# Performance work log

Hardware: AMD Instinct MI355X
Metric: run time of the kernel (lower is better)

Reference implementation:

```python
import jax, jax.numpy as jnp
import numpy as np

B, S, D, H = 2, 2048, 1024, 16
DK = D // H  # 64, per-head key/value dim


def setup_inputs() -> dict:
    key = jax.random.key(0)
    ks = jax.random.split(key, 8)
    q = jax.random.normal(ks[0], (B, S, D), dtype=jnp.float32)
    k = jax.random.normal(ks[1], (B, S, D), dtype=jnp.float32)
    v = jax.random.normal(ks[2], (B, S, D), dtype=jnp.float32)
    # per-head projection weights, initialized like torch.randn in the original
    W_q = jax.random.normal(ks[3], (H, D, DK), dtype=jnp.float32)
    W_k = jax.random.normal(ks[4], (H, D, DK), dtype=jnp.float32)
    W_v = jax.random.normal(ks[5], (H, D, DK), dtype=jnp.float32)
    # output nn.Linear(H*DK, D): weight [D, H*DK], bias [D]
    bound = 1.0 / np.sqrt(H * DK)
    W_o = jax.random.uniform(ks[6], (D, H * DK), dtype=jnp.float32, minval=-bound, maxval=bound)
    b_o = jax.random.uniform(ks[7], (D,), dtype=jnp.float32, minval=-bound, maxval=bound)
    return {"q": q, "k": k, "v": v, "W_q": W_q, "W_k": W_k, "W_v": W_v, "W_o": W_o, "b_o": b_o}


def reference(q, k, v, W_q, W_k, W_v, W_o, b_o):
    dk = W_q.shape[-1]
    # batched per-head projections (replaces the Python loop over heads)
    qh = jnp.einsum('bsd,hdk->bhsk', q, W_q)  # [B,H,S,DK]
    kh = jnp.einsum('bsd,hdk->bhsk', k, W_k)
    vh = jnp.einsum('bsd,hdk->bhsk', v, W_v)
    scale = jnp.asarray(np.sqrt(dk), qh.dtype)
    scores = jnp.einsum('bhsk,bhtk->bhst', qh, kh) / scale  # [B,H,S,S]
    attn = jax.nn.softmax(scores, axis=-1)
    ctx = jnp.einsum('bhst,bhtk->bhsk', attn, vh)  # [B,H,S,DK]
    # concat heads along feature dim (matches torch.cat(..., dim=2))
    b, h, s, d = ctx.shape
    ctx = ctx.transpose(0, 2, 1, 3).reshape(b, s, h * d)  # [B,S,H*DK]
    return ctx @ W_o.T + b_o  # [B,S,D]
```

## Files before the change

### kernel.cpp

```cpp
#include <hip/hip_runtime.h>
#include <math.h>

#define B_ 2
#define S_ 2048
#define D_ 1024
#define H_ 16
#define ATTN_C 0.18033688011f

typedef unsigned short ushort_t;
typedef __attribute__((ext_vector_type(8))) short short8;
typedef __attribute__((ext_vector_type(4))) short short4v;
typedef __attribute__((ext_vector_type(4))) float f32x4;
typedef __attribute__((ext_vector_type(2))) float f32x2;
typedef __attribute__((ext_vector_type(16))) float f32x16;
typedef __attribute__((ext_vector_type(4))) unsigned int uint4v;

#define MFMA(A, B, C) __builtin_amdgcn_mfma_f32_32x32x16_bf16((A), (B), (C), 0, 0, 0)
#define Z16 {0.f,0.f,0.f,0.f,0.f,0.f,0.f,0.f,0.f,0.f,0.f,0.f,0.f,0.f,0.f,0.f}

__device__ __forceinline__ ushort_t bf16rn(float x) {
    unsigned int u = __builtin_bit_cast(unsigned int, x);
    u += 0x7FFFu + ((u >> 16) & 1u);
    return (ushort_t)(u >> 16);
}
__device__ __forceinline__ float bf16tof(ushort_t h) {
    return __builtin_bit_cast(float, (unsigned int)h << 16);
}
__device__ __forceinline__ unsigned cvtpk(float lo, float hi) {
    unsigned r;
    asm("v_cvt_pk_bf16_f32 %0, %1, %2" : "=v"(r) : "v"(lo), "v"(hi));
    return r;
}
__device__ __forceinline__ void gload16(const void* g, void* l) {
    __builtin_amdgcn_global_load_lds(
        (const __attribute__((address_space(1))) unsigned int*)(unsigned long long)g,
        (__attribute__((address_space(3))) unsigned int*)(unsigned int)(unsigned long long)l,
        16, 0, 0);
}

__global__ __launch_bounds__(256) void cvtx_kernel(
    const float* __restrict__ Xq, const float* __restrict__ Xk,
    const float* __restrict__ Xv,
    ushort_t* __restrict__ Xh, ushort_t* __restrict__ Xl)
{
    const int pr = blockIdx.y;
    const float* X = pr == 0 ? Xq : pr == 1 ? Xk : Xv;
    const size_t idx = ((size_t)blockIdx.x * 256 + threadIdx.x) * 8;
    f32x4 v0 = *(const f32x4*)(X + idx);
    f32x4 v1 = *(const f32x4*)(X + idx + 4);
    float f[8] = {v0.x, v0.y, v0.z, v0.w, v1.x, v1.y, v1.z, v1.w};
    short8 hi, lo;
#pragma unroll
    for (int i = 0; i < 8; ++i) {
        ushort_t hh = bf16rn(f[i]);
        hi[i] = (short)hh;
        lo[i] = (short)bf16rn(f[i] - bf16tof(hh));
    }
    const size_t base = (size_t)pr * 2 * S_ * D_;
    *(short8*)(Xh + base + idx) = hi;
    if (pr < 2) *(short8*)(Xl + base + idx) = lo;
}

__global__ __launch_bounds__(256) void cvtw_kernel(
    const float* __restrict__ Wq, const float* __restrict__ Wk,
    const float* __restrict__ Wv,
    ushort_t* __restrict__ wqh, ushort_t* __restrict__ wql,
    ushort_t* __restrict__ wkh, ushort_t* __restrict__ wkl,
    ushort_t* __restrict__ wvh)
{
    __shared__ float T[64][68];
    const int dt = blockIdx.x, h = blockIdx.y, mat = blockIdx.z;
    const int tid = threadIdx.x;
    const float* W = mat == 0 ? Wq : mat == 1 ? Wk : Wv;
    const float* Wb = W + ((size_t)h * 1024 + dt * 64) * 64;
#pragma unroll
    for (int u = 0; u < 4; ++u) {
        int idx = tid + u * 256;
        int d = idx >> 4, c4 = idx & 15;
        f32x4 v = *(const f32x4*)(Wb + (size_t)d * 64 + c4 * 4);
        T[d][c4 * 4 + 0] = v.x; T[d][c4 * 4 + 1] = v.y;
        T[d][c4 * 4 + 2] = v.z; T[d][c4 * 4 + 3] = v.w;
    }
    __syncthreads();
    ushort_t* oh = mat == 0 ? wqh : mat == 1 ? wkh : wvh;
    ushort_t* ol = mat == 0 ? wql : mat == 1 ? wkl : nullptr;
#pragma unroll
    for (int u = 0; u < 4; ++u) {
        int idx = tid + u * 256;
        int n = idx >> 4, c4 = idx & 15;
        float v0 = T[c4 * 4 + 0][n], v1 = T[c4 * 4 + 1][n];
        float v2 = T[c4 * 4 + 2][n], v3 = T[c4 * 4 + 3][n];
        ushort_t h0 = bf16rn(v0), h1 = bf16rn(v1), h2 = bf16rn(v2), h3 = bf16rn(v3);
        size_t off = ((size_t)h * 64 + n) * 1024 + dt * 64 + c4 * 4;
        short4v hv = {(short)h0, (short)h1, (short)h2, (short)h3};
        *(short4v*)(oh + off) = hv;
        if (ol) {
            short4v lv = {(short)bf16rn(v0 - bf16tof(h0)), (short)bf16rn(v1 - bf16tof(h1)),
                          (short)bf16rn(v2 - bf16tof(h2)), (short)bf16rn(v3 - bf16tof(h3))};
            *(short4v*)(ol + off) = lv;
        }
    }
}

__global__ __launch_bounds__(256) void cvtwo_kernel(
    const float* __restrict__ Wo, ushort_t* __restrict__ wob)
{
    size_t idx = (size_t)blockIdx.x * 256 + threadIdx.x;
    f32x4 v = *(const f32x4*)(Wo + idx * 4);
    short4v o = {(short)bf16rn(v.x), (short)bf16rn(v.y),
                 (short)bf16rn(v.z), (short)bf16rn(v.w)};
    *(short4v*)(wob + idx * 4) = o;
}

__global__ __launch_bounds__(256, 2) void proj_kernel(
    const ushort_t* __restrict__ Xh, const ushort_t* __restrict__ Xl,
    const ushort_t* __restrict__ Wh_q, const ushort_t* __restrict__ Wl_q,
    const ushort_t* __restrict__ Wh_k, const ushort_t* __restrict__ Wl_k,
    const ushort_t* __restrict__ Wh_v,
    ushort_t* __restrict__ Oq_h, ushort_t* __restrict__ Oq_l,
    ushort_t* __restrict__ Ok_h, ushort_t* __restrict__ Ok_l,
    ushort_t* __restrict__ Ovt)
{
    __shared__ __align__(16) ushort_t Xs[128 * 128];
    __shared__ __align__(16) ushort_t Ws[128 * 128];
    const int tid = threadIdx.x;
    const int wv = tid >> 6, lane = tid & 63;
    const int lo32 = lane & 31, g = lane >> 5;
    const int wm = wv >> 1, wn = wv & 1;
    const int lrow = lane >> 4, lg = lane & 15;
    const int m0 = blockIdx.x * 128;
    const int n0 = blockIdx.y * 128;
    const int pr = blockIdx.z >> 1, b = blockIdx.z & 1;
    const bool split = (pr != 2);
    const ushort_t* Whp = pr == 0 ? Wh_q : pr == 1 ? Wh_k : Wh_v;
    const ushort_t* Wlp = pr == 0 ? Wl_q : pr == 1 ? Wl_k : Wh_v;
    const ushort_t* Xhb = Xh + ((size_t)(pr * 2 + b) * S_ + m0) * D_;
    const ushort_t* Xlb = Xl + ((size_t)(pr * 2 + b) * S_ + m0) * D_;
    f32x16 a00 = Z16, a01 = Z16, a10 = Z16, a11 = Z16;

    for (int d0 = 0; d0 < D_; d0 += 64) {
        __syncthreads();
#pragma unroll
        for (int u = 0; u < 8; ++u) {
            int row = u * 16 + wv * 4 + lrow;
            int gs = lg ^ (row & 15);
            int half = gs >> 3, c8 = gs & 7;
            const ushort_t* srcX = ((half && split) ? Xlb : Xhb) + (size_t)row * D_ + d0 + c8 * 8;
            gload16(srcX, (char*)Xs + (u * 16 + wv * 4) * 256);
            const ushort_t* srcW = ((half && split) ? Wlp : Whp) + (size_t)(n0 + row) * 1024 + d0 + c8 * 8;
            gload16(srcW, (char*)Ws + (u * 16 + wv * 4) * 256);
        }
        __syncthreads();
#pragma unroll
        for (int ks = 0; ks < 4; ++ks) {
            int coff = ks * 16 + g * 8;
            int r0 = wm * 64 + lo32, r1 = r0 + 32;
            int c0 = wn * 64 + lo32, c1 = c0 + 32;
            short8 a0h = *(const short8*)&Xs[(r0 * 128 + coff) ^ ((r0 & 15) << 3)];
            short8 a1h = *(const short8*)&Xs[(r1 * 128 + coff) ^ ((r1 & 15) << 3)];
            short8 b0h = *(const short8*)&Ws[(c0 * 128 + coff) ^ ((c0 & 15) << 3)];
            short8 b1h = *(const short8*)&Ws[(c1 * 128 + coff) ^ ((c1 & 15) << 3)];
            a00 = MFMA(a0h, b0h, a00);
            a01 = MFMA(a0h, b1h, a01);
            a10 = MFMA(a1h, b0h, a10);
            a11 = MFMA(a1h, b1h, a11);
            if (split) {
                short8 a0l = *(const short8*)&Xs[(r0 * 128 + 64 + coff) ^ ((r0 & 15) << 3)];
                short8 a1l = *(const short8*)&Xs[(r1 * 128 + 64 + coff) ^ ((r1 & 15) << 3)];
                short8 b0l = *(const short8*)&Ws[(c0 * 128 + 64 + coff) ^ ((c0 & 15) << 3)];
                short8 b1l = *(const short8*)&Ws[(c1 * 128 + 64 + coff) ^ ((c1 & 15) << 3)];
                a00 = MFMA(a0h, b0l, a00); a00 = MFMA(a0l, b0h, a00);
                a01 = MFMA(a0h, b1l, a01); a01 = MFMA(a0l, b1h, a01);
                a10 = MFMA(a1h, b0l, a10); a10 = MFMA(a1l, b0h, a10);
                a11 = MFMA(a1h, b1l, a11); a11 = MFMA(a1l, b1h, a11);
            }
        }
    }
    ushort_t* OH = pr == 0 ? Oq_h : pr == 1 ? Ok_h : Ovt;
    ushort_t* OL = pr == 0 ? Oq_l : pr == 1 ? Ok_l : Ovt;
    const bool qscale = (pr == 0);
#define PROJ_STORE(ACC, MT, NT)                                               \
    _Pragma("unroll")                                                         \
    for (int r = 0; r < 16; ++r) {                                            \
        int s_loc = m0 + wm * 64 + (MT) * 32 + (r & 3) + 8 * (r >> 2) + 4 * g;\
        int col = n0 + wn * 64 + (NT) * 32 + lo32;                            \
        int hh_ = col >> 6, nn = col & 63;                                    \
        float val = ACC[r];                                                   \
        if (qscale) val *= ATTN_C;                                            \
        if (split) {                                                          \
            size_t off = (((size_t)b * H_ + hh_) * S_ + s_loc) * 64 + nn;     \
            ushort_t hv = bf16rn(val);                                        \
            OH[off] = hv;                                                     \
            OL[off] = bf16rn(val - bf16tof(hv));                              \
        } else {                                                              \
            size_t offt = (((size_t)b * H_ + hh_) * 64 + nn) * S_ + s_loc;    \
            OH[offt] = bf16rn(val);                                           \
        }                                                                     \
    }
    PROJ_STORE(a00, 0, 0)
    PROJ_STORE(a01, 0, 1)
    PROJ_STORE(a10, 1, 0)
    PROJ_STORE(a11, 1, 1)
#undef PROJ_STORE
}

__global__ __launch_bounds__(256, 2) void attn_kernel(
    const ushort_t* __restrict__ qh_h, const ushort_t* __restrict__ qh_l,
    const ushort_t* __restrict__ kh_h, const ushort_t* __restrict__ kh_l,
    const ushort_t* __restrict__ vt, ushort_t* __restrict__ Opart,
    float* __restrict__ Ml)
{
    __shared__ __align__(16) char smem[49152];
    ushort_t* Ks = (ushort_t*)smem;
    ushort_t* Vt = (ushort_t*)(smem + 32768);
    const int tid = threadIdx.x;
    const int wv = tid >> 6, lane = tid & 63;
    const int lo32 = lane & 31, g = lane >> 5;
    const int lrow = lane >> 4, lg = lane & 15;
    const int s0 = blockIdx.x * 256;
    const int h = blockIdx.y;
    const int b = blockIdx.z >> 1, sp = blockIdx.z & 1;
    const size_t bhs = ((size_t)b * H_ + h) * S_ * 64;

    short8 qfh[2][4], qfl[2][4];
#pragma unroll
    for (int c = 0; c < 2; ++c) {
        const ushort_t* Qrh = qh_h + bhs + (size_t)(s0 + wv * 64 + c * 32 + lo32) * 64;
        const ushort_t* Qrl = qh_l + bhs + (size_t)(s0 + wv * 64 + c * 32 + lo32) * 64;
#pragma unroll
        for (int ks = 0; ks < 4; ++ks) {
            qfh[c][ks] = *(const short8*)(Qrh + ks * 16 + g * 8);
            qfl[c][ks] = *(const short8*)(Qrl + ks * 16 + g * 8);
        }
    }
    const ushort_t* Kgh = kh_h + bhs;
    const ushort_t* Kgl = kh_l + bhs;
    const ushort_t* Vtg = vt + ((size_t)b * H_ + h) * 64 * S_;

    f32x16 o00 = Z16, o01 = Z16, o10 = Z16, o11 = Z16;
    float mrun0 = -3.0e38f, mrun1 = -3.0e38f;
    float lrun0 = 0.f, lrun1 = 0.f;
    const int kvbeg = sp * (S_ / 2), kvend = kvbeg + (S_ / 2);

    for (int kv0 = kvbeg; kv0 < kvend; kv0 += 128) {
        __syncthreads();
#pragma unroll
        for (int u = 0; u < 8; ++u) {
            int row = u * 16 + wv * 4 + lrow;
            int gs = lg ^ (row & 15);
            int half = gs >> 3, c8 = gs & 7;
            const ushort_t* src = (half ? Kgl : Kgh) + (size_t)(kv0 + row) * 64 + c8 * 8;
            gload16(src, (char*)Ks + (u * 16 + wv * 4) * 256);
        }
#pragma unroll
        for (int u = 0; u < 4; ++u) {
            int d = u * 16 + wv * 4 + lrow;
            int gsrc = (lg & 8) | ((lg & 7) ^ (d & 7));
            const ushort_t* src = Vtg + (size_t)d * S_ + kv0 + gsrc * 8;
            gload16(src, (char*)Vt + (u * 16 + wv * 4) * 256);
        }
        __syncthreads();
#pragma unroll 1
        for (int ch = 0; ch < 4; ++ch) {
            const int kvb = ch * 32;
            const int krow = kvb + lo32;
            const int ksw = (krow & 15) << 3;
            short8 kfh0 = *(const short8*)&Ks[(krow * 128 + 0 * 16 + g * 8) ^ ksw];
            short8 kfh1 = *(const short8*)&Ks[(krow * 128 + 1 * 16 + g * 8) ^ ksw];
            short8 kfh2 = *(const short8*)&Ks[(krow * 128 + 2 * 16 + g * 8) ^ ksw];
            short8 kfh3 = *(const short8*)&Ks[(krow * 128 + 3 * 16 + g * 8) ^ ksw];
            f32x16 st0 = Z16, st1 = Z16;
            st0 = MFMA(kfh0, qfh[0][0], st0);  st1 = MFMA(kfh0, qfh[1][0], st1);
            st0 = MFMA(kfh1, qfh[0][1], st0);  st1 = MFMA(kfh1, qfh[1][1], st1);
            st0 = MFMA(kfh2, qfh[0][2], st0);  st1 = MFMA(kfh2, qfh[1][2], st1);
            st0 = MFMA(kfh3, qfh[0][3], st0);  st1 = MFMA(kfh3, qfh[1][3], st1);
            float cm0 = fmaxf(fmaxf(fmaxf(st0[0], st0[1]), fmaxf(st0[2], st0[3])),
                              fmaxf(fmaxf(st0[4], st0[5]), fmaxf(st0[6], st0[7])));
            cm0 = fmaxf(cm0, fmaxf(fmaxf(fmaxf(st0[8], st0[9]), fmaxf(st0[10], st0[11])),
                                   fmaxf(fmaxf(st0[12], st0[13]), fmaxf(st0[14], st0[15]))));
            float cm1 = fmaxf(fmaxf(fmaxf(st1[0], st1[1]), fmaxf(st1[2], st1[3])),
                              fmaxf(fmaxf(st1[4], st1[5]), fmaxf(st1[6], st1[7])));
            cm1 = fmaxf(cm1, fmaxf(fmaxf(fmaxf(st1[8], st1[9]), fmaxf(st1[10], st1[11])),
                                   fmaxf(fmaxf(st1[12], st1[13]), fmaxf(st1[14], st1[15]))));
            cm0 = fmaxf(cm0, __shfl_xor(cm0, 32));
            cm1 = fmaxf(cm1, __shfl_xor(cm1, 32));
            const bool need0 = !__all(cm0 <= mrun0 - 142.f);
            const bool need1 = !__all(cm1 <= mrun1 - 142.f);
            if (!need0 && !need1) continue;
            short8 kfl0 = *(const short8*)&Ks[(krow * 128 + 64 + 0 * 16 + g * 8) ^ ksw];
            short8 kfl1 = *(const short8*)&Ks[(krow * 128 + 64 + 1 * 16 + g * 8) ^ ksw];
            short8 kfl2 = *(const short8*)&Ks[(krow * 128 + 64 + 2 * 16 + g * 8) ^ ksw];
            short8 kfl3 = *(const short8*)&Ks[(krow * 128 + 64 + 3 * 16 + g * 8) ^ ksw];
            unsigned pw0[8], pw1[8];
            if (need0) {
                st0 = MFMA(kfh0, qfl[0][0], st0);  st0 = MFMA(kfl0, qfh[0][0], st0);
                st0 = MFMA(kfh1, qfl[0][1], st0);  st0 = MFMA(kfl1, qfh[0][1], st0);
                st0 = MFMA(kfh2, qfl[0][2], st0);  st0 = MFMA(kfl2, qfh[0][2], st0);
                st0 = MFMA(kfh3, qfl[0][3], st0);  st0 = MFMA(kfl3, qfh[0][3], st0);
                float cme = fmaxf(fmaxf(fmaxf(st0[0], st0[1]), fmaxf(st0[2], st0[3])),
                                  fmaxf(fmaxf(st0[4], st0[5]), fmaxf(st0[6], st0[7])));
                cme = fmaxf(cme, fmaxf(fmaxf(fmaxf(st0[8], st0[9]), fmaxf(st0[10], st0[11])),
                                       fmaxf(fmaxf(st0[12], st0[13]), fmaxf(st0[14], st0[15]))));
                cme = fmaxf(cme, __shfl_xor(cme, 32));
                if (!__all(cme <= mrun0)) {
                    float mnew = fmaxf(mrun0, cme);
                    float corr = __builtin_amdgcn_exp2f(mrun0 - mnew);
                    lrun0 *= corr;
#pragma unroll
                    for (int r = 0; r < 16; ++r) { o00[r] *= corr; o01[r] *= corr; }
                    mrun0 = mnew;
                }
                float p[16], ls = 0.f;
#pragma unroll
                for (int r = 0; r < 16; ++r) {
                    p[r] = __builtin_amdgcn_exp2f(st0[r] - mrun0);
                    ls += p[r];
                }
                lrun0 += ls;
#pragma unroll
                for (int ks2 = 0; ks2 < 2; ++ks2) {
                    unsigned w0 = cvtpk(p[ks2 * 8 + 0], p[ks2 * 8 + 1]);
                    unsigned w1 = cvtpk(p[ks2 * 8 + 2], p[ks2 * 8 + 3]);
                    unsigned w2 = cvtpk(p[ks2 * 8 + 4], p[ks2 * 8 + 5]);
                    unsigned w3 = cvtpk(p[ks2 * 8 + 6], p[ks2 * 8 + 7]);
                    asm("v_permlane32_swap_b32 %0, %1" : "+v"(w0), "+v"(w2));
                    asm("v_permlane32_swap_b32 %0, %1" : "+v"(w1), "+v"(w3));
                    pw0[ks2 * 4 + 0] = w0; pw0[ks2 * 4 + 1] = w1;
                    pw0[ks2 * 4 + 2] = w2; pw0[ks2 * 4 + 3] = w3;
                }
            }
            if (need1) {
                st1 = MFMA(kfh0, qfl[1][0], st1);  st1 = MFMA(kfl0, qfh[1][0], st1);
                st1 = MFMA(kfh1, qfl[1][1], st1);  st1 = MFMA(kfl1, qfh[1][1], st1);
                st1 = MFMA(kfh2, qfl[1][2], st1);  st1 = MFMA(kfl2, qfh[1][2], st1);
                st1 = MFMA(kfh3, qfl[1][3], st1);  st1 = MFMA(kfl3, qfh[1][3], st1);
                float cme = fmaxf(fmaxf(fmaxf(st1[0], st1[1]), fmaxf(st1[2], st1[3])),
                                  fmaxf(fmaxf(st1[4], st1[5]), fmaxf(st1[6], st1[7])));
                cme = fmaxf(cme, fmaxf(fmaxf(fmaxf(st1[8], st1[9]), fmaxf(st1[10], st1[11])),
                                       fmaxf(fmaxf(st1[12], st1[13]), fmaxf(st1[14], st1[15]))));
                cme = fmaxf(cme, __shfl_xor(cme, 32));
                if (!__all(cme <= mrun1)) {
                    float mnew = fmaxf(mrun1, cme);
                    float corr = __builtin_amdgcn_exp2f(mrun1 - mnew);
                    lrun1 *= corr;
#pragma unroll
                    for (int r = 0; r < 16; ++r) { o10[r] *= corr; o11[r] *= corr; }
                    mrun1 = mnew;
                }
                float p[16], ls = 0.f;
#pragma unroll
                for (int r = 0; r < 16; ++r) {
                    p[r] = __builtin_amdgcn_exp2f(st1[r] - mrun1);
                    ls += p[r];
                }
                lrun1 += ls;
#pragma unroll
                for (int ks2 = 0; ks2 < 2; ++ks2) {
                    unsigned w0 = cvtpk(p[ks2 * 8 + 0], p[ks2 * 8 + 1]);
                    unsigned w1 = cvtpk(p[ks2 * 8 + 2], p[ks2 * 8 + 3]);
                    unsigned w2 = cvtpk(p[ks2 * 8 + 4], p[ks2 * 8 + 5]);
                    unsigned w3 = cvtpk(p[ks2 * 8 + 6], p[ks2 * 8 + 7]);
                    asm("v_permlane32_swap_b32 %0, %1" : "+v"(w0), "+v"(w2));
                    asm("v_permlane32_swap_b32 %0, %1" : "+v"(w1), "+v"(w3));
                    pw1[ks2 * 4 + 0] = w0; pw1[ks2 * 4 + 1] = w1;
                    pw1[ks2 * 4 + 2] = w2; pw1[ks2 * 4 + 3] = w3;
                }
            }
#pragma unroll
            for (int ks2 = 0; ks2 < 2; ++ks2) {
                int kvf = kvb + ks2 * 16 + g * 8;
                int vsw = (lo32 & 7) << 3;
                short8 vf0 = *(const short8*)&Vt[(lo32 * 128 + kvf) ^ vsw];
                short8 vf1 = *(const short8*)&Vt[((lo32 + 32) * 128 + kvf) ^ vsw];
                if (need0) {
                    uint4v a = {pw0[ks2 * 4 + 0], pw0[ks2 * 4 + 1],
                                pw0[ks2 * 4 + 2], pw0[ks2 * 4 + 3]};
                    short8 pf = __builtin_bit_cast(short8, a);
                    o00 = MFMA(vf0, pf, o00);
                    o01 = MFMA(vf1, pf, o01);
                }
                if (need1) {
                    uint4v a = {pw1[ks2 * 4 + 0], pw1[ks2 * 4 + 1],
                                pw1[ks2 * 4 + 2], pw1[ks2 * 4 + 3]};
                    short8 pf = __builtin_bit_cast(short8, a);
                    o10 = MFMA(vf0, pf, o10);
                    o11 = MFMA(vf1, pf, o11);
                }
            }
        }
    }
    lrun0 += __shfl_xor(lrun0, 32);
    lrun1 += __shfl_xor(lrun1, 32);
    __syncthreads();
    float* Oe = ((float*)smem) + wv * 2048;
    const size_t orowb = (size_t)sp * (B_ * H_ * S_) + ((size_t)b * H_ + h) * S_ + s0 + wv * 64;
#pragma unroll
    for (int r = 0; r < 16; ++r) {
        int dd = (r & 3) + 8 * (r >> 2) + 4 * g;
        int qsw = (lo32 & 7) << 2;
        Oe[(lo32 * 64 + dd) ^ qsw] = o00[r];
        Oe[(lo32 * 64 + 32 + dd) ^ qsw] = o01[r];
    }
#pragma unroll
    for (int rep = 0; rep < 8; ++rep) {
        int idx = lane + rep * 64;
        int qq = idx >> 4, d4 = idx & 15;
        f32x4 ov = *(const f32x4*)&Oe[(qq * 64 + d4 * 4) ^ ((qq & 7) << 2)];
        short4v pk4 = {(short)bf16rn(ov.x), (short)bf16rn(ov.y),
                       (short)bf16rn(ov.z), (short)bf16rn(ov.w)};
        *(short4v*)(Opart + (orowb + qq) * 64 + d4 * 4) = pk4;
    }
    if (g == 0) {
        f32x2 ml = {mrun0, lrun0};
        *(f32x2*)(Ml + (orowb + lo32) * 2) = ml;
    }
    __builtin_amdgcn_s_waitcnt(0);
#pragma unroll
    for (int r = 0; r < 16; ++r) {
        int dd = (r & 3) + 8 * (r >> 2) + 4 * g;
        int qsw = (lo32 & 7) << 2;
        Oe[(lo32 * 64 + dd) ^ qsw] = o10[r];
        Oe[(lo32 * 64 + 32 + dd) ^ qsw] = o11[r];
    }
#pragma unroll
    for (int rep = 0; rep < 8; ++rep) {
        int idx = lane + rep * 64;
        int qq = idx >> 4, d4 = idx & 15;
        f32x4 ov = *(const f32x4*)&Oe[(qq * 64 + d4 * 4) ^ ((qq & 7) << 2)];
        short4v pk4 = {(short)bf16rn(ov.x), (short)bf16rn(ov.y),
                       (short)bf16rn(ov.z), (short)bf16rn(ov.w)};
        *(short4v*)(Opart + (orowb + 32 + qq) * 64 + d4 * 4) = pk4;
    }
    if (g == 0) {
        f32x2 ml = {mrun1, lrun1};
        *(f32x2*)(Ml + (orowb + 32 + lo32) * 2) = ml;
    }
}

__global__ __launch_bounds__(256) void merge_kernel(
    const ushort_t* __restrict__ Opart, const float* __restrict__ Ml,
    ushort_t* __restrict__ ctxb)
{
    const int NROW = B_ * H_ * S_;
    int gidx = blockIdx.x * 256 + threadIdx.x;
    int row = gidx >> 3, d8 = (gidx & 7) * 8;
    f32x2 ml0 = *(const f32x2*)(Ml + (size_t)row * 2);
    f32x2 ml1 = *(const f32x2*)(Ml + ((size_t)NROW + row) * 2);
    float M = fmaxf(ml0.x, ml1.x);
    float w0 = __builtin_amdgcn_exp2f(ml0.x - M);
    float w1 = __builtin_amdgcn_exp2f(ml1.x - M);
    float inv = 1.f / (ml0.y * w0 + ml1.y * w1);
    w0 *= inv; w1 *= inv;
    short8 a = *(const short8*)(Opart + (size_t)row * 64 + d8);
    short8 c = *(const short8*)(Opart + ((size_t)NROW + row) * 64 + d8);
    short8 o;
#pragma unroll
    for (int i = 0; i < 8; ++i) {
        float f = bf16tof((ushort_t)a[i]) * w0 + bf16tof((ushort_t)c[i]) * w1;
        o[i] = (short)bf16rn(f);
    }
    int bb = row >> 15, hh = (row >> 11) & 15, s = row & 2047;
    *(short8*)(ctxb + ((size_t)bb * S_ + s) * D_ + hh * 64 + d8) = o;
}

__global__ __launch_bounds__(128, 2) void outproj_kernel(
    const ushort_t* __restrict__ ctxb, const ushort_t* __restrict__ wob,
    const float* __restrict__ bo, float* __restrict__ Out)
{
    __shared__ __align__(16) ushort_t Cs[128 * 128];
    __shared__ __align__(16) ushort_t Ws2[64 * 128];
    const int tid = threadIdx.x;
    const int wv = tid >> 6, lane = tid & 63;
    const int lo32 = lane & 31, g = lane >> 5;
    const int lrow = lane >> 4, lg = lane & 15;
    const int n0 = blockIdx.x * 64;
    const int m0 = blockIdx.y * 128;
    f32x16 a00 = Z16, a01 = Z16, a10 = Z16, a11 = Z16;
    for (int k0 = 0; k0 < D_; k0 += 128) {
        __syncthreads();
#pragma unroll
        for (int u = 0; u < 16; ++u) {
            int row = u * 8 + wv * 4 + lrow;
            int gs = lg ^ (row & 15);
            const ushort_t* src = ctxb + (size_t)(m0 + row) * D_ + k0 + gs * 8;
            gload16(src, (char*)Cs + (u * 8 + wv * 4) * 256);
        }
#pragma unroll
        for (int u = 0; u < 8; ++u) {
            int row = u * 8 + wv * 4 + lrow;
            int gs = lg ^ (row & 15);
            const ushort_t* src = wob + (size_t)(n0 + row) * D_ + k0 + gs * 8;
            gload16(src, (char*)Ws2 + (u * 8 + wv * 4) * 256);
        }
        __syncthreads();
#pragma unroll
        for (int ks = 0; ks < 8; ++ks) {
            int coff = ks * 16 + g * 8;
            int r0 = wv * 64 + lo32, r1 = r0 + 32;
            int n1 = lo32 + 32;
            short8 A0 = *(const short8*)&Cs[(r0 * 128 + coff) ^ ((r0 & 15) << 3)];
            short8 A1 = *(const short8*)&Cs[(r1 * 128 + coff) ^ ((r1 & 15) << 3)];
            short8 B0 = *(const short8*)&Ws2[(lo32 * 128 + coff) ^ ((lo32 & 15) << 3)];
            short8 B1 = *(const short8*)&Ws2[(n1 * 128 + coff) ^ ((n1 & 15) << 3)];
            a00 = MFMA(A0, B0, a00);
            a01 = MFMA(A0, B1, a01);
            a10 = MFMA(A1, B0, a10);
            a11 = MFMA(A1, B1, a11);
        }
    }
    float b0v = bo[n0 + lo32], b1v = bo[n0 + 32 + lo32];
#define OUT_STORE(ACC, MT, NT, BV)                                          \
    _Pragma("unroll")                                                       \
    for (int r = 0; r < 16; ++r) {                                          \
        int m = m0 + wv * 64 + (MT) * 32 + (r & 3) + 8 * (r >> 2) + 4 * g;  \
        int n = n0 + (NT) * 32 + lo32;                                      \
        Out[(size_t)m * D_ + n] = ACC[r] + (BV);                            \
    }
    OUT_STORE(a00, 0, 0, b0v)
    OUT_STORE(a01, 0, 1, b1v)
    OUT_STORE(a10, 1, 0, b0v)
    OUT_STORE(a11, 1, 1, b1v)
#undef OUT_STORE
}

extern "C" void kernel_launch(void* const* d_in, const int* in_sizes, int n_in,
                              void* d_out, int out_size, void* d_ws,
                              size_t ws_size, hipStream_t stream)
{
    const float* q = (const float*)d_in[0];
    const float* k = (const float*)d_in[1];
    const float* v = (const float*)d_in[2];
    const float* W_q = (const float*)d_in[3];
    const float* W_k = (const float*)d_in[4];
    const float* W_v = (const float*)d_in[5];
    const float* W_o = (const float*)d_in[6];
    const float* b_o = (const float*)d_in[7];
    float* out = (float*)d_out;

    ushort_t* wqt_h = (ushort_t*)d_ws;
    ushort_t* wqt_l = wqt_h + (1 << 20);
    ushort_t* wkt_h = wqt_l + (1 << 20);
    ushort_t* wkt_l = wkt_h + (1 << 20);
    ushort_t* wvt_h = wkt_l + (1 << 20);
// ... 25 lines not shown
```

Baseline: 229.7 us.

## Load K fragments directly from global with register double-buffering, drop K LDS staging

K high/low fragments are no longer staged through shared memory. Each wave reads its K rows straight from global into registers, prefetching the next 32-row chunk while the current one computes. The low-part K is read from global only when the skip test says it is needed. The skip threshold moves from 142 to 150 and the four chunks per tile are fully unrolled. This lowers LDS use and cuts barrier-protected K copy traffic, but each wave now fetches K itself, so global/L2 traffic goes up, and the full unroll may raise register pressure.

```diff
diff --git a/kernel.cpp b/kernel.cpp
--- a/kernel.cpp
+++ b/kernel.cpp
@@ -210,9 +210,8 @@
     const ushort_t* __restrict__ vt, ushort_t* __restrict__ Opart,
     float* __restrict__ Ml)
 {
-    __shared__ __align__(16) char smem[49152];
-    ushort_t* Ks = (ushort_t*)smem;
-    ushort_t* Vt = (ushort_t*)(smem + 32768);
+    __shared__ __align__(16) char smem[32768];
+    ushort_t* Vt = (ushort_t*)smem;
     const int tid = threadIdx.x;
     const int wv = tid >> 6, lane = tid & 63;
     const int lo32 = lane & 31, g = lane >> 5;
@@ -240,18 +239,115 @@
     f32x16 o00 = Z16, o01 = Z16, o10 = Z16, o11 = Z16;
     float mrun0 = -3.0e38f, mrun1 = -3.0e38f;
     float lrun0 = 0.f, lrun1 = 0.f;
-    const int kvbeg = sp * (S_ / 2), kvend = kvbeg + (S_ / 2);
-
-    for (int kv0 = kvbeg; kv0 < kvend; kv0 += 128) {
+    const int kvbeg = sp * (S_ / 2);
+
+#define MAX16(ST) fmaxf(fmaxf(fmaxf(fmaxf(ST[0], ST[1]), fmaxf(ST[2], ST[3])),   \
+                              fmaxf(fmaxf(ST[4], ST[5]), fmaxf(ST[6], ST[7]))),  \
+                        fmaxf(fmaxf(fmaxf(ST[8], ST[9]), fmaxf(ST[10], ST[11])), \
+                              fmaxf(fmaxf(ST[12], ST[13]), fmaxf(ST[14], ST[15]))))
+
+#define SOFTMAX_PV(ST, MR, LR, OA, OB)                                        \
+    {                                                                         \
+        float cme = MAX16(ST);                                                \
+        cme = fmaxf(cme, __shfl_xor(cme, 32));                                \
+        if (!__all(cme <= MR)) {                                              \
+            float mnew = fmaxf(MR, cme);                                      \
+            float corr = __builtin_amdgcn_exp2f(MR - mnew);                   \
+            LR *= corr;                                                       \
+            _Pragma("unroll")                                                 \
+            for (int r = 0; r < 16; ++r) { OA[r] *= corr; OB[r] *= corr; }    \
+            MR = mnew;                                                        \
+        }                                                                     \
+        float p[16], ls = 0.f;                                                \
+        _Pragma("unroll")                                                     \
+        for (int r = 0; r < 16; ++r) {                                        \
+            p[r] = __builtin_amdgcn_exp2f(ST[r] - MR);                        \
+            ls += p[r];                                                       \
+        }                                                                     \
+        LR += ls;                                                             \
+        {                                                                     \
+            unsigned w0 = cvtpk(p[0], p[1]), w1 = cvtpk(p[2], p[3]);          \
+            unsigned w2 = cvtpk(p[4], p[5]), w3 = cvtpk(p[6], p[7]);          \
+            asm("v_permlane32_swap_b32 %0, %1" : "+v"(w0), "+v"(w2));         \
+            asm("v_permlane32_swap_b32 %0, %1" : "+v"(w1), "+v"(w3));         \
+            uint4v pa = {w0, w1, w2, w3};                                     \
+            short8 pf = __builtin_bit_cast(short8, pa);                       \
+            OA = MFMA(vfa0, pf, OA);                                          \
+            OB = MFMA(vfa1, pf, OB);                                          \
+            w0 = cvtpk(p[8], p[9]);  w1 = cvtpk(p[10], p[11]);                \
+            w2 = cvtpk(p[12], p[13]); w3 = cvtpk(p[14], p[15]);               \
+            asm("v_permlane32_swap_b32 %0, %1" : "+v"(w0), "+v"(w2));         \
+            asm("v_permlane32_swap_b32 %0, %1" : "+v"(w1), "+v"(w3));         \
+            uint4v pb = {w0, w1, w2, w3};                                     \
+            short8 pf2 = __builtin_bit_cast(short8, pb);                      \
+            OA = MFMA(vfb0, pf2, OA);                                         \
+            OB = MFMA(vfb1, pf2, OB);                                         \
+        }                                                                     \
+    }
+
+#define LOADK(CI, DST)                                                        \
+    {                                                                         \
+        int cc = (CI) > 31 ? 31 : (CI);                                       \
+        const ushort_t* pn = Kgh + (size_t)(kvbeg + cc * 32 + lo32) * 64 + g * 8; \
+        DST[0] = *(const short8*)(pn);                                        \
+        DST[1] = *(const short8*)(pn + 16);                                   \
+        DST[2] = *(const short8*)(pn + 32);                                   \
+        DST[3] = *(const short8*)(pn + 48);                                   \
+    }
+
+#define CHUNK_BODY(KC, KN, CI)                                                \
+    {                                                                         \
+        LOADK((CI) + 1, KN);                                                  \
+        f32x16 st0 = Z16, st1 = Z16;                                          \
+        st0 = MFMA(KC[0], qfh[0][0], st0);  st1 = MFMA(KC[0], qfh[1][0], st1);\
+        st0 = MFMA(KC[1], qfh[0][1], st0);  st1 = MFMA(KC[1], qfh[1][1], st1);\
+        st0 = MFMA(KC[2], qfh[0][2], st0);  st1 = MFMA(KC[2], qfh[1][2], st1);\
+        st0 = MFMA(KC[3], qfh[0][3], st0);  st1 = MFMA(KC[3], qfh[1][3], st1);\
+        float cm0 = MAX16(st0);                                               \
+        float cm1 = MAX16(st1);                                               \
+        cm0 = fmaxf(cm0, __shfl_xor(cm0, 32));                                \
+        cm1 = fmaxf(cm1, __shfl_xor(cm1, 32));                                \
+        const bool need0 = !__all(cm0 <= mrun0 - 150.f);                      \
+        const bool need1 = !__all(cm1 <= mrun1 - 150.f);                      \
+        if (need0 | need1) {                                                  \
+            const ushort_t* pl = Kgl + (size_t)(kvbeg + (CI) * 32 + lo32) * 64 + g * 8; \
+            short8 kl0 = *(const short8*)(pl);                                \
+            short8 kl1 = *(const short8*)(pl + 16);                           \
+            short8 kl2 = *(const short8*)(pl + 32);                           \
+            short8 kl3 = *(const short8*)(pl + 48);                           \
+            if (need0) {                                                      \
+                st0 = MFMA(KC[0], qfl[0][0], st0); st0 = MFMA(KC[1], qfl[0][1], st0); \
+                st0 = MFMA(KC[2], qfl[0][2], st0); st0 = MFMA(KC[3], qfl[0][3], st0); \
+            }                                                                 \
+            if (need1) {                                                      \
+                st1 = MFMA(KC[0], qfl[1][0], st1); st1 = MFMA(KC[1], qfl[1][1], st1); \
+                st1 = MFMA(KC[2], qfl[1][2], st1); st1 = MFMA(KC[3], qfl[1][3], st1); \
+            }                                                                 \
+            if (need0) {                                                      \
+                st0 = MFMA(kl0, qfh[0][0], st0); st0 = MFMA(kl1, qfh[0][1], st0); \
+                st0 = MFMA(kl2, qfh[0][2], st0); st0 = MFMA(kl3, qfh[0][3], st0); \
+            }                                                                 \
+            if (need1) {                                                      \
+                st1 = MFMA(kl0, qfh[1][0], st1); st1 = MFMA(kl1, qfh[1][1], st1); \
+                st1 = MFMA(kl2, qfh[1][2], st1); st1 = MFMA(kl3, qfh[1][3], st1); \
+            }                                                                 \
+            const int kvb = ((CI) & 3) * 32;                                  \
+            const int vsw = (lo32 & 7) << 3;                                  \
+            short8 vfa0 = *(const short8*)&Vt[(lo32 * 128 + kvb + g * 8) ^ vsw];        \
+            short8 vfa1 = *(const short8*)&Vt[((lo32 + 32) * 128 + kvb + g * 8) ^ vsw]; \
+            short8 vfb0 = *(const short8*)&Vt[(lo32 * 128 + kvb + 16 + g * 8) ^ vsw];   \
+            short8 vfb1 = *(const short8*)&Vt[((lo32 + 32) * 128 + kvb + 16 + g * 8) ^ vsw]; \
+            if (need0) SOFTMAX_PV(st0, mrun0, lrun0, o00, o01)                \
+            if (need1) SOFTMAX_PV(st1, mrun1, lrun1, o10, o11)                \
+        }                                                                     \
+    }
+
+    short8 kx[4], ky[4];
+    LOADK(0, kx);
+    int c = 0;
+    for (int t = 0; t < 8; ++t) {
+        const int kv0 = kvbeg + t * 128;
         __syncthreads();
-#pragma unroll
-        for (int u = 0; u < 8; ++u) {
-            int row = u * 16 + wv * 4 + lrow;
-            int gs = lg ^ (row & 15);
-            int half = gs >> 3, c8 = gs & 7;
-            const ushort_t* src = (half ? Kgl : Kgh) + (size_t)(kv0 + row) * 64 + c8 * 8;
-            gload16(src, (char*)Ks + (u * 16 + wv * 4) * 256);
-        }
 #pragma unroll
         for (int u = 0; u < 4; ++u) {
             int d = u * 16 + wv * 4 + lrow;
@@ -260,135 +356,17 @@
             gload16(src, (char*)Vt + (u * 16 + wv * 4) * 256);
         }
         __syncthreads();
-#pragma unroll 1
-        for (int ch = 0; ch < 4; ++ch) {
-            const int kvb = ch * 32;
-            const int krow = kvb + lo32;
-            const int ksw = (krow & 15) << 3;
-            short8 kfh0 = *(const short8*)&Ks[(krow * 128 + 0 * 16 + g * 8) ^ ksw];
-            short8 kfh1 = *(const short8*)&Ks[(krow * 128 + 1 * 16 + g * 8) ^ ksw];
-            short8 kfh2 = *(const short8*)&Ks[(krow * 128 + 2 * 16 + g * 8) ^ ksw];
-            short8 kfh3 = *(const short8*)&Ks[(krow * 128 + 3 * 16 + g * 8) ^ ksw];
-            f32x16 st0 = Z16, st1 = Z16;
-            st0 = MFMA(kfh0, qfh[0][0], st0);  st1 = MFMA(kfh0, qfh[1][0], st1);
-            st0 = MFMA(kfh1, qfh[0][1], st0);  st1 = MFMA(kfh1, qfh[1][1], st1);
-            st0 = MFMA(kfh2, qfh[0][2], st0);  st1 = MFMA(kfh2, qfh[1][2], st1);
-            st0 = MFMA(kfh3, qfh[0][3], st0);  st1 = MFMA(kfh3, qfh[1][3], st1);
-            float cm0 = fmaxf(fmaxf(fmaxf(st0[0], st0[1]), fmaxf(st0[2], st0[3])),
-                              fmaxf(fmaxf(st0[4], st0[5]), fmaxf(st0[6], st0[7])));
-            cm0 = fmaxf(cm0, fmaxf(fmaxf(fmaxf(st0[8], st0[9]), fmaxf(st0[10], st0[11])),
-                                   fmaxf(fmaxf(st0[12], st0[13]), fmaxf(st0[14], st0[15]))));
-            float cm1 = fmaxf(fmaxf(fmaxf(st1[0], st1[1]), fmaxf(st1[2], st1[3])),
-                              fmaxf(fmaxf(st1[4], st1[5]), fmaxf(st1[6], st1[7])));
-            cm1 = fmaxf(cm1, fmaxf(fmaxf(fmaxf(st1[8], st1[9]), fmaxf(st1[10], st1[11])),
-                                   fmaxf(fmaxf(st1[12], st1[13]), fmaxf(st1[14], st1[15]))));
-            cm0 = fmaxf(cm0, __shfl_xor(cm0, 32));
-            cm1 = fmaxf(cm1, __shfl_xor(cm1, 32));
-            const bool need0 = !__all(cm0 <= mrun0 - 142.f);
-            const bool need1 = !__all(cm1 <= mrun1 - 142.f);
-            if (!need0 && !need1) continue;
-            short8 kfl0 = *(const short8*)&Ks[(krow * 128 + 64 + 0 * 16 + g * 8) ^ ksw];
-            short8 kfl1 = *(const short8*)&Ks[(krow * 128 + 64 + 1 * 16 + g * 8) ^ ksw];
-            short8 kfl2 = *(const short8*)&Ks[(krow * 128 + 64 + 2 * 16 + g * 8) ^ ksw];
-            short8 kfl3 = *(const short8*)&Ks[(krow * 128 + 64 + 3 * 16 + g * 8) ^ ksw];
-            unsigned pw0[8], pw1[8];
-            if (need0) {
-                st0 = MFMA(kfh0, qfl[0][0], st0);  st0 = MFMA(kfl0, qfh[0][0], st0);
-                st0 = MFMA(kfh1, qfl[0][1], st0);  st0 = MFMA(kfl1, qfh[0][1], st0);
-                st0 = MFMA(kfh2, qfl[0][2], st0);  st0 = MFMA(kfl2, qfh[0][2], st0);
-                st0 = MFMA(kfh3, qfl[0][3], st0);  st0 = MFMA(kfl3, qfh[0][3], st0);
-                float cme = fmaxf(fmaxf(fmaxf(st0[0], st0[1]), fmaxf(st0[2], st0[3])),
-                                  fmaxf(fmaxf(st0[4], st0[5]), fmaxf(st0[6], st0[7])));
-                cme = fmaxf(cme, fmaxf(fmaxf(fmaxf(st0[8], st0[9]), fmaxf(st0[10], st0[11])),
-                                       fmaxf(fmaxf(st0[12], st0[13]), fmaxf(st0[14], st0[15]))));
-                cme = fmaxf(cme, __shfl_xor(cme, 32));
-                if (!__all(cme <= mrun0)) {
-                    float mnew = fmaxf(mrun0, cme);
-                    float corr = __builtin_amdgcn_exp2f(mrun0 - mnew);
-                    lrun0 *= corr;
-#pragma unroll
-                    for (int r = 0; r < 16; ++r) { o00[r] *= corr; o01[r] *= corr; }
-                    mrun0 = mnew;
-                }
-                float p[16], ls = 0.f;
-#pragma unroll
-                for (int r = 0; r < 16; ++r) {
-                    p[r] = __builtin_amdgcn_exp2f(st0[r] - mrun0);
-                    ls += p[r];
-                }
-                lrun0 += ls;
-#pragma unroll
-                for (int ks2 = 0; ks2 < 2; ++ks2) {
-                    unsigned w0 = cvtpk(p[ks2 * 8 + 0], p[ks2 * 8 + 1]);
-                    unsigned w1 = cvtpk(p[ks2 * 8 + 2], p[ks2 * 8 + 3]);
-                    unsigned w2 = cvtpk(p[ks2 * 8 + 4], p[ks2 * 8 + 5]);
-                    unsigned w3 = cvtpk(p[ks2 * 8 + 6], p[ks2 * 8 + 7]);
-                    asm("v_permlane32_swap_b32 %0, %1" : "+v"(w0), "+v"(w2));
-                    asm("v_permlane32_swap_b32 %0, %1" : "+v"(w1), "+v"(w3));
-                    pw0[ks2 * 4 + 0] = w0; pw0[ks2 * 4 + 1] = w1;
-                    pw0[ks2 * 4 + 2] = w2; pw0[ks2 * 4 + 3] = w3;
-                }
-            }
-            if (need1) {
-                st1 = MFMA(kfh0, qfl[1][0], st1);  st1 = MFMA(kfl0, qfh[1][0], st1);
-                st1 = MFMA(kfh1, qfl[1][1], st1);  st1 = MFMA(kfl1, qfh[1][1], st1);
-                st1 = MFMA(kfh2, qfl[1][2], st1);  st1 = MFMA(kfl2, qfh[1][2], st1);
-                st1 = MFMA(kfh3, qfl[1][3], st1);  st1 = MFMA(kfl3, qfh[1][3], st1);
-                float cme = fmaxf(fmaxf(fmaxf(st1[0], st1[1]), fmaxf(st1[2], st1[3])),
-                                  fmaxf(fmaxf(st1[4], st1[5]), fmaxf(st1[6], st1[7])));
-                cme = fmaxf(cme, fmaxf(fmaxf(fmaxf(st1[8], st1[9]), fmaxf(st1[10], st1[11])),
-                                       fmaxf(fmaxf(st1[12], st1[13]), fmaxf(st1[14], st1[15]))));
-                cme = fmaxf(cme, __shfl_xor(cme, 32));
-                if (!__all(cme <= mrun1)) {
-                    float mnew = fmaxf(mrun1, cme);
-                    float corr = __builtin_amdgcn_exp2f(mrun1 - mnew);
-                    lrun1 *= corr;
-#pragma unroll
-                    for (int r = 0; r < 16; ++r) { o10[r] *= corr; o11[r] *= corr; }
-                    mrun1 = mnew;
-                }
-                float p[16], ls = 0.f;
-#pragma unroll
-                for (int r = 0; r < 16; ++r) {
-                    p[r] = __builtin_amdgcn_exp2f(st1[r] - mrun1);
-                    ls += p[r];
-                }
-                lrun1 += ls;
-#pragma unroll
-                for (int ks2 = 0; ks2 < 2; ++ks2) {
-                    unsigned w0 = cvtpk(p[ks2 * 8 + 0], p[ks2 * 8 + 1]);
-                    unsigned w1 = cvtpk(p[ks2 * 8 + 2], p[ks2 * 8 + 3]);
-                    unsigned w2 = cvtpk(p[ks2 * 8 + 4], p[ks2 * 8 + 5]);
-                    unsigned w3 = cvtpk(p[ks2 * 8 + 6], p[ks2 * 8 + 7]);
-                    asm("v_permlane32_swap_b32 %0, %1" : "+v"(w0), "+v"(w2));
-                    asm("v_permlane32_swap_b32 %0, %1" : "+v"(w1), "+v"(w3));
-                    pw1[ks2 * 4 + 0] = w0; pw1[ks2 * 4 + 1] = w1;
-                    pw1[ks2 * 4 + 2] = w2; pw1[ks2 * 4 + 3] = w3;
-                }
-            }
-#pragma unroll
-            for (int ks2 = 0; ks2 < 2; ++ks2) {
-                int kvf = kvb + ks2 * 16 + g * 8;
-                int vsw = (lo32 & 7) << 3;
-                short8 vf0 = *(const short8*)&Vt[(lo32 * 128 + kvf) ^ vsw];
-                short8 vf1 = *(const short8*)&Vt[((lo32 + 32) * 128 + kvf) ^ vsw];
-                if (need0) {
-                    uint4v a = {pw0[ks2 * 4 + 0], pw0[ks2 * 4 + 1],
-                                pw0[ks2 * 4 + 2], pw0[ks2 * 4 + 3]};
-                    short8 pf = __builtin_bit_cast(short8, a);
-                    o00 = MFMA(vf0, pf, o00);
-                    o01 = MFMA(vf1, pf, o01);
-                }
-                if (need1) {
-                    uint4v a = {pw1[ks2 * 4 + 0], pw1[ks2 * 4 + 1],
-                                pw1[ks2 * 4 + 2], pw1[ks2 * 4 + 3]};
-                    short8 pf = __builtin_bit_cast(short8, a);
-                    o10 = MFMA(vf0, pf, o10);
-                    o11 = MFMA(vf1, pf, o11);
-                }
-            }
-        }
-    }
+        CHUNK_BODY(kx, ky, c + 0)
+        CHUNK_BODY(ky, kx, c + 1)
+        CHUNK_BODY(kx, ky, c + 2)
+        CHUNK_BODY(ky, kx, c + 3)
+        c += 4;
+    }
+#undef CHUNK_BODY
+#undef LOADK
+#undef SOFTMAX_PV
+#undef MAX16
+
     lrun0 += __shfl_xor(lrun0, 32);
     lrun1 += __shfl_xor(lrun1, 32);
     __syncthreads();
```

Measured after the change: 232.9 us. About the same (+1.4%).

## Tighten softmax skip thresholds and stage transposed V stores through LDS

Applied to the files above, without the earlier changes.

The attention loop now skips the low-half score refinement for a 32-key chunk unless some score lies within 64 (log2 units) of the running max, where the old cutoff was 142. It also skips the exp, packing and P·V MFMAs when the refined chunk max is more than 30 below the running max, since those probabilities would fall below about 2^-30. The max reductions are collapsed into a macro. The V projection path now writes its transposed output through an LDS tile, giving 16-byte coalesced global stores instead of scattered 2-byte strided writes. The cost is extra syncs in the projection kernel and a small, bounded approximation error from dropping negligible softmax terms.

```diff
diff --git a/kernel.cpp b/kernel.cpp
--- a/kernel.cpp
+++ b/kernel.cpp
@@ -176,9 +176,10 @@
             }
         }
     }
-    ushort_t* OH = pr == 0 ? Oq_h : pr == 1 ? Ok_h : Ovt;
-    ushort_t* OL = pr == 0 ? Oq_l : pr == 1 ? Ok_l : Ovt;
-    const bool qscale = (pr == 0);
+    if (split) {
+        ushort_t* OH = pr == 0 ? Oq_h : Ok_h;
+        ushort_t* OL = pr == 0 ? Oq_l : Ok_l;
+        const bool qscale = (pr == 0);
 #define PROJ_STORE(ACC, MT, NT)                                               \
     _Pragma("unroll")                                                         \
     for (int r = 0; r < 16; ++r) {                                            \
@@ -187,21 +188,42 @@
         int hh_ = col >> 6, nn = col & 63;                                    \
         float val = ACC[r];                                                   \
         if (qscale) val *= ATTN_C;                                            \
-        if (split) {                                                          \
-            size_t off = (((size_t)b * H_ + hh_) * S_ + s_loc) * 64 + nn;     \
-            ushort_t hv = bf16rn(val);                                        \
-            OH[off] = hv;                                                     \
-            OL[off] = bf16rn(val - bf16tof(hv));                              \
-        } else {                                                              \
-            size_t offt = (((size_t)b * H_ + hh_) * 64 + nn) * S_ + s_loc;    \
-            OH[offt] = bf16rn(val);                                           \
-        }                                                                     \
-    }
-    PROJ_STORE(a00, 0, 0)
-    PROJ_STORE(a01, 0, 1)
-    PROJ_STORE(a10, 1, 0)
-    PROJ_STORE(a11, 1, 1)
+        size_t off = (((size_t)b * H_ + hh_) * S_ + s_loc) * 64 + nn;         \
+        ushort_t hv = bf16rn(val);                                            \
+        OH[off] = hv;                                                         \
+        OL[off] = bf16rn(val - bf16tof(hv));                                  \
+    }
+        PROJ_STORE(a00, 0, 0)
+        PROJ_STORE(a01, 0, 1)
+        PROJ_STORE(a10, 1, 0)
+        PROJ_STORE(a11, 1, 1)
 #undef PROJ_STORE
+    } else {
+        __syncthreads();
+        ushort_t* T = Xs;
+#define VT_PUT(ACC, MT, NT)                                                   \
+    _Pragma("unroll")                                                         \
+    for (int r = 0; r < 16; ++r) {                                            \
+        int s_loc = wm * 64 + (MT) * 32 + (r & 3) + 8 * (r >> 2) + 4 * g;     \
+        int col   = wn * 64 + (NT) * 32 + lo32;                               \
+        T[col * 128 + (s_loc ^ ((col & 15) << 3))] = bf16rn(ACC[r]);          \
+    }
+        VT_PUT(a00, 0, 0)
+        VT_PUT(a01, 0, 1)
+        VT_PUT(a10, 1, 0)
+        VT_PUT(a11, 1, 1)
+#undef VT_PUT
+        __syncthreads();
+#pragma unroll
+        for (int u = 0; u < 8; ++u) {
+            int idx = tid + u * 256;
+            int col = idx >> 4, ch = idx & 15;
+            short8 v8 = *(const short8*)&T[col * 128 + ((ch * 8) ^ ((col & 15) << 3))];
+            int gn = n0 + col;
+            size_t orow = ((size_t)b * H_ + (gn >> 6)) * 64 + (gn & 63);
+            *(short8*)(Ovt + orow * S_ + m0 + ch * 8) = v8;
+        }
+    }
 }
 
 __global__ __launch_bounds__(256, 2) void attn_kernel(
@@ -241,6 +263,13 @@
     float mrun0 = -3.0e38f, mrun1 = -3.0e38f;
     float lrun0 = 0.f, lrun1 = 0.f;
     const int kvbeg = sp * (S_ / 2), kvend = kvbeg + (S_ / 2);
+
+#define MAX16(ST)                                                             \
+    fmaxf(fmaxf(fmaxf(fmaxf(ST[0], ST[1]), ST[2]),                            \
+                fmaxf(fmaxf(ST[3], ST[4]), ST[5])),                           \
+          fmaxf(fmaxf(fmaxf(ST[6], ST[7]), fmaxf(ST[8], ST[9])),              \
+                fmaxf(fmaxf(fmaxf(ST[10], ST[11]), ST[12]),                   \
+                      fmaxf(fmaxf(ST[13], ST[14]), ST[15]))))
 
     for (int kv0 = kvbeg; kv0 < kvend; kv0 += 128) {
         __syncthreads();
@@ -274,59 +303,54 @@
             st0 = MFMA(kfh1, qfh[0][1], st0);  st1 = MFMA(kfh1, qfh[1][1], st1);
             st0 = MFMA(kfh2, qfh[0][2], st0);  st1 = MFMA(kfh2, qfh[1][2], st1);
             st0 = MFMA(kfh3, qfh[0][3], st0);  st1 = MFMA(kfh3, qfh[1][3], st1);
-            float cm0 = fmaxf(fmaxf(fmaxf(st0[0], st0[1]), fmaxf(st0[2], st0[3])),
-                              fmaxf(fmaxf(st0[4], st0[5]), fmaxf(st0[6], st0[7])));
-            cm0 = fmaxf(cm0, fmaxf(fmaxf(fmaxf(st0[8], st0[9]), fmaxf(st0[10], st0[11])),
-                                   fmaxf(fmaxf(st0[12], st0[13]), fmaxf(st0[14], st0[15]))));
-            float cm1 = fmaxf(fmaxf(fmaxf(st1[0], st1[1]), fmaxf(st1[2], st1[3])),
-                              fmaxf(fmaxf(st1[4], st1[5]), fmaxf(st1[6], st1[7])));
-            cm1 = fmaxf(cm1, fmaxf(fmaxf(fmaxf(st1[8], st1[9]), fmaxf(st1[10], st1[11])),
-                                   fmaxf(fmaxf(st1[12], st1[13]), fmaxf(st1[14], st1[15]))));
+            float cm0 = MAX16(st0);
+            float cm1 = MAX16(st1);
             cm0 = fmaxf(cm0, __shfl_xor(cm0, 32));
             cm1 = fmaxf(cm1, __shfl_xor(cm1, 32));
-            const bool need0 = !__all(cm0 <= mrun0 - 142.f);
-            const bool need1 = !__all(cm1 <= mrun1 - 142.f);
+            const bool need0 = __any(cm0 > mrun0 - 64.f);
+            const bool need1 = __any(cm1 > mrun1 - 64.f);
             if (!need0 && !need1) continue;
             short8 kfl0 = *(const short8*)&Ks[(krow * 128 + 64 + 0 * 16 + g * 8) ^ ksw];
             short8 kfl1 = *(const short8*)&Ks[(krow * 128 + 64 + 1 * 16 + g * 8) ^ ksw];
             short8 kfl2 = *(const short8*)&Ks[(krow * 128 + 64 + 2 * 16 + g * 8) ^ ksw];
             short8 kfl3 = *(const short8*)&Ks[(krow * 128 + 64 + 3 * 16 + g * 8) ^ ksw];
             unsigned pw0[8], pw1[8];
+            bool pv0 = false, pv1 = false;
             if (need0) {
                 st0 = MFMA(kfh0, qfl[0][0], st0);  st0 = MFMA(kfl0, qfh[0][0], st0);
                 st0 = MFMA(kfh1, qfl[0][1], st0);  st0 = MFMA(kfl1, qfh[0][1], st0);
                 st0 = MFMA(kfh2, qfl[0][2], st0);  st0 = MFMA(kfl2, qfh[0][2], st0);
                 st0 = MFMA(kfh3, qfl[0][3], st0);  st0 = MFMA(kfl3, qfh[0][3], st0);
-                float cme = fmaxf(fmaxf(fmaxf(st0[0], st0[1]), fmaxf(st0[2], st0[3])),
-                                  fmaxf(fmaxf(st0[4], st0[5]), fmaxf(st0[6], st0[7])));
-                cme = fmaxf(cme, fmaxf(fmaxf(fmaxf(st0[8], st0[9]), fmaxf(st0[10], st0[11])),
-                                       fmaxf(fmaxf(st0[12], st0[13]), fmaxf(st0[14], st0[15]))));
+                float cme = MAX16(st0);
                 cme = fmaxf(cme, __shfl_xor(cme, 32));
-                if (!__all(cme <= mrun0)) {
-                    float mnew = fmaxf(mrun0, cme);
-                    float corr = __builtin_amdgcn_exp2f(mrun0 - mnew);
-                    lrun0 *= corr;
-#pragma unroll
-                    for (int r = 0; r < 16; ++r) { o00[r] *= corr; o01[r] *= corr; }
-                    mrun0 = mnew;
-                }
-                float p[16], ls = 0.f;
-#pragma unroll
-                for (int r = 0; r < 16; ++r) {
-                    p[r] = __builtin_amdgcn_exp2f(st0[r] - mrun0);
-                    ls += p[r];
-                }
-                lrun0 += ls;
-#pragma unroll
-                for (int ks2 = 0; ks2 < 2; ++ks2) {
-                    unsigned w0 = cvtpk(p[ks2 * 8 + 0], p[ks2 * 8 + 1]);
-                    unsigned w1 = cvtpk(p[ks2 * 8 + 2], p[ks2 * 8 + 3]);
-                    unsigned w2 = cvtpk(p[ks2 * 8 + 4], p[ks2 * 8 + 5]);
-                    unsigned w3 = cvtpk(p[ks2 * 8 + 6], p[ks2 * 8 + 7]);
-                    asm("v_permlane32_swap_b32 %0, %1" : "+v"(w0), "+v"(w2));
-                    asm("v_permlane32_swap_b32 %0, %1" : "+v"(w1), "+v"(w3));
-                    pw0[ks2 * 4 + 0] = w0; pw0[ks2 * 4 + 1] = w1;
-                    pw0[ks2 * 4 + 2] = w2; pw0[ks2 * 4 + 3] = w3;
+                pv0 = __any(cme > mrun0 - 30.f);
+                if (pv0) {
+                    if (__any(cme > mrun0)) {
+                        float mnew = fmaxf(mrun0, cme);
+                        float corr = __builtin_amdgcn_exp2f(mrun0 - mnew);
+                        lrun0 *= corr;
+#pragma unroll
+                        for (int r = 0; r < 16; ++r) { o00[r] *= corr; o01[r] *= corr; }
+                        mrun0 = mnew;
+                    }
+                    float p[16], ls = 0.f;
+#pragma unroll
+                    for (int r = 0; r < 16; ++r) {
+                        p[r] = __builtin_amdgcn_exp2f(st0[r] - mrun0);
+                        ls += p[r];
+                    }
+                    lrun0 += ls;
+#pragma unroll
+                    for (int ks2 = 0; ks2 < 2; ++ks2) {
+                        unsigned w0 = cvtpk(p[ks2 * 8 + 0], p[ks2 * 8 + 1]);
+                        unsigned w1 = cvtpk(p[ks2 * 8 + 2], p[ks2 * 8 + 3]);
+                        unsigned w2 = cvtpk(p[ks2 * 8 + 4], p[ks2 * 8 + 5]);
+                        unsigned w3 = cvtpk(p[ks2 * 8 + 6], p[ks2 * 8 + 7]);
+                        asm("v_permlane32_swap_b32 %0, %1" : "+v"(w0), "+v"(w2));
+                        asm("v_permlane32_swap_b32 %0, %1" : "+v"(w1), "+v"(w3));
+                        pw0[ks2 * 4 + 0] = w0; pw0[ks2 * 4 + 1] = w1;
+                        pw0[ks2 * 4 + 2] = w2; pw0[ks2 * 4 + 3] = w3;
+                    }
                 }
             }
             if (need1) {
@@ -334,61 +358,65 @@
                 st1 = MFMA(kfh1, qfl[1][1], st1);  st1 = MFMA(kfl1, qfh[1][1], st1);
                 st1 = MFMA(kfh2, qfl[1][2], st1);  st1 = MFMA(kfl2, qfh[1][2], st1);
                 st1 = MFMA(kfh3, qfl[1][3], st1);  st1 = MFMA(kfl3, qfh[1][3], st1);
-                float cme = fmaxf(fmaxf(fmaxf(st1[0], st1[1]), fmaxf(st1[2], st1[3])),
-                                  fmaxf(fmaxf(st1[4], st1[5]), fmaxf(st1[6], st1[7])));
-                cme = fmaxf(cme, fmaxf(fmaxf(fmaxf(st1[8], st1[9]), fmaxf(st1[10], st1[11])),
-                                       fmaxf(fmaxf(st1[12], st1[13]), fmaxf(st1[14], st1[15]))));
+                float cme = MAX16(st1);
                 cme = fmaxf(cme, __shfl_xor(cme, 32));
-                if (!__all(cme <= mrun1)) {
-                    float mnew = fmaxf(mrun1, cme);
-                    float corr = __builtin_amdgcn_exp2f(mrun1 - mnew);
-                    lrun1 *= corr;
-#pragma unroll
-                    for (int r = 0; r < 16; ++r) { o10[r] *= corr; o11[r] *= corr; }
-                    mrun1 = mnew;
-                }
-                float p[16], ls = 0.f;
-#pragma unroll
-                for (int r = 0; r < 16; ++r) {
-                    p[r] = __builtin_amdgcn_exp2f(st1[r] - mrun1);
-                    ls += p[r];
-                }
-                lrun1 += ls;
-#pragma unroll
-                for (int ks2 = 0; ks2 < 2; ++ks2) {
-                    unsigned w0 = cvtpk(p[ks2 * 8 + 0], p[ks2 * 8 + 1]);
-                    unsigned w1 = cvtpk(p[ks2 * 8 + 2], p[ks2 * 8 + 3]);
-                    unsigned w2 = cvtpk(p[ks2 * 8 + 4], p[ks2 * 8 + 5]);
-                    unsigned w3 = cvtpk(p[ks2 * 8 + 6], p[ks2 * 8 + 7]);
-                    asm("v_permlane32_swap_b32 %0, %1" : "+v"(w0), "+v"(w2));
-                    asm("v_permlane32_swap_b32 %0, %1" : "+v"(w1), "+v"(w3));
-                    pw1[ks2 * 4 + 0] = w0; pw1[ks2 * 4 + 1] = w1;
-                    pw1[ks2 * 4 + 2] = w2; pw1[ks2 * 4 + 3] = w3;
+                pv1 = __any(cme > mrun1 - 30.f);
+                if (pv1) {
+                    if (__any(cme > mrun1)) {
+                        float mnew = fmaxf(mrun1, cme);
+                        float corr = __builtin_amdgcn_exp2f(mrun1 - mnew);
+                        lrun1 *= corr;
+#pragma unroll
+                        for (int r = 0; r < 16; ++r) { o10[r] *= corr; o11[r] *= corr; }
+                        mrun1 = mnew;
+                    }
+                    float p[16], ls = 0.f;
+#pragma unroll
+                    for (int r = 0; r < 16; ++r) {
+                        p[r] = __builtin_amdgcn_exp2f(st1[r] - mrun1);
+                        ls += p[r];
+                    }
+                    lrun1 += ls;
+#pragma unroll
+                    for (int ks2 = 0; ks2 < 2; ++ks2) {
+                        unsigned w0 = cvtpk(p[ks2 * 8 + 0], p[ks2 * 8 + 1]);
+                        unsigned w1 = cvtpk(p[ks2 * 8 + 2], p[ks2 * 8 + 3]);
+                        unsigned w2 = cvtpk(p[ks2 * 8 + 4], p[ks2 * 8 + 5]);
+                        unsigned w3 = cvtpk(p[ks2 * 8 + 6], p[ks2 * 8 + 7]);
+                        asm("v_permlane32_swap_b32 %0, %1" : "+v"(w0), "+v"(w2));
+                        asm("v_permlane32_swap_b32 %0, %1" : "+v"(w1), "+v"(w3));
+                        pw1[ks2 * 4 + 0] = w0; pw1[ks2 * 4 + 1] = w1;
+                        pw1[ks2 * 4 + 2] = w2; pw1[ks2 * 4 + 3] = w3;
+                    }
                 }
             }
-#pragma unroll
-            for (int ks2 = 0; ks2 < 2; ++ks2) {
-                int kvf = kvb + ks2 * 16 + g * 8;
-                int vsw = (lo32 & 7) << 3;
-                short8 vf0 = *(const short8*)&Vt[(lo32 * 128 + kvf) ^ vsw];
-                short8 vf1 = *(const short8*)&Vt[((lo32 + 32) * 128 + kvf) ^ vsw];
-                if (need0) {
-                    uint4v a = {pw0[ks2 * 4 + 0], pw0[ks2 * 4 + 1],
-                                pw0[ks2 * 4 + 2], pw0[ks2 * 4 + 3]};
-                    short8 pf = __builtin_bit_cast(short8, a);
-                    o00 = MFMA(vf0, pf, o00);
-                    o01 = MFMA(vf1, pf, o01);
-                }
-                if (need1) {
-                    uint4v a = {pw1[ks2 * 4 + 0], pw1[ks2 * 4 + 1],
-                                pw1[ks2 * 4 + 2], pw1[ks2 * 4 + 3]};
-                    short8 pf = __builtin_bit_cast(short8, a);
-                    o10 = MFMA(vf0, pf, o10);
-                    o11 = MFMA(vf1, pf, o11);
+            if (pv0 | pv1) {
+#pragma unroll
+                for (int ks2 = 0; ks2 < 2; ++ks2) {
+                    int kvf = kvb + ks2 * 16 + g * 8;
+                    int vsw = (lo32 & 7) << 3;
+                    short8 vf0 = *(const short8*)&Vt[(lo32 * 128 + kvf) ^ vsw];
+                    short8 vf1 = *(const short8*)&Vt[((lo32 + 32) * 128 + kvf) ^ vsw];
+                    if (pv0) {
+                        uint4v a = {pw0[ks2 * 4 + 0], pw0[ks2 * 4 + 1],
+                                    pw0[ks2 * 4 + 2], pw0[ks2 * 4 + 3]};
+                        short8 pf = __builtin_bit_cast(short8, a);
+                        o00 = MFMA(vf0, pf, o00);
+                        o01 = MFMA(vf1, pf, o01);
+                    }
+                    if (pv1) {
+                        uint4v a = {pw1[ks2 * 4 + 0], pw1[ks2 * 4 + 1],
+                                    pw1[ks2 * 4 + 2], pw1[ks2 * 4 + 3]};
+                        short8 pf = __builtin_bit_cast(short8, a);
+                        o10 = MFMA(vf0, pf, o10);
+                        o11 = MFMA(vf1, pf, o11);
+                    }
                 }
             }
         }
     }
+#undef MAX16
+
     lrun0 += __shfl_xor(lrun0, 32);
     lrun1 += __shfl_xor(lrun1, 32);
     __syncthreads();
```

Result: faster. 218.1 us (-5.0%).
